# Kernel tuning notes

Measured on AMD Instinct MI355X. Metric: run time of the kernel, lower is better.

The kernel has to match this reference:

```python
import jax, jax.numpy as jnp
import numpy as np
from jax import lax

S, B, XD, AD, ZD, K, H = 128, 32, 1024, 8, 4, 3, 50
CN = 32 * 3 * 3
DN = ('NCHW', 'OIHW', 'NCHW')


def setup_inputs():
    key = jax.random.key(0)
    ks = jax.random.split(key, 20)
    g = lambda k, sh, s=0.1: jax.random.normal(k, sh, dtype=jnp.float32) * s
    z = lambda n: jnp.zeros((n,), jnp.float32)
    return {
        'x': jax.random.uniform(ks[0], (S, B, XD), dtype=jnp.float32),
        'eps': jax.random.normal(ks[1], (S, B, AD), dtype=jnp.float32),
        'Wc0': g(ks[2], (32, 1, 3, 3)), 'bc0': z(32),
        'Wc1': g(ks[3], (32, 32, 3, 3)), 'bc1': z(32),
        'Wc2': g(ks[4], (32, 32, 3, 3)), 'bc2': z(32),
        'Wm': g(ks[5], (AD, CN)), 'bm': z(AD),
        'Wlv': g(ks[6], (AD, CN)), 'blv': z(AD),
        'Wd': g(ks[7], (CN, AD)), 'bd': z(CN),
        'Wt0': g(ks[8], (32, 32, 3, 3)), 'bt0': z(32),
        'Wt1': g(ks[9], (32, 32, 3, 3)), 'bt1': z(32),
        'Wt2': g(ks[10], (32, 32, 3, 3)), 'bt2': z(32),
        'Wg': g(ks[11], (32, 1, 1, 1)), 'bg': z(1),
        'A': jnp.tile(jnp.eye(ZD, dtype=jnp.float32)[None], (K, 1, 1)),
        'Bm': g(ks[12], (K, ZD, AD), 0.05),
        'Cm': g(ks[13], (K, AD, ZD), 0.05),
        'a_init': jnp.zeros((1, AD), jnp.float32),
        'W_ih': g(ks[14], (4 * H, AD)), 'W_hh': g(ks[15], (4 * H, H)),
        'b_ih': z(4 * H), 'b_hh': z(4 * H),
        'Wa': g(ks[16], (K, H)), 'ba': z(K),
    }


def _conv(h, W, b):
    y = lax.conv_general_dilated(h, W, (2, 2), 'VALID', dimension_numbers=DN)
    return y + b[None, :, None, None]


def _convT(h, W, b, op):
    # PyTorch ConvTranspose2d(k=3, stride=2, padding=0, output_padding=op)
    Wf = jnp.transpose(jnp.flip(W, (2, 3)), (1, 0, 2, 3))
    pad = (2, 2 + op)
    y = lax.conv_general_dilated(h, Wf, (1, 1), [pad, pad], lhs_dilation=(2, 2), dimension_numbers=DN)
    return y + b[None, :, None, None]


def _forward(x, eps, Wc0, bc0, Wc1, bc1, Wc2, bc2, Wm, bm, Wlv, blv, Wd, bd,
             Wt0, bt0, Wt1, bt1, Wt2, bt2, Wg, bg, A, Bm, Cm, a_init,
             W_ih, W_hh, b_ih, b_hh, Wa, ba):
    relu, sig = jax.nn.relu, jax.nn.sigmoid
    # ---- encode: x -> a ----
    xf = x.reshape(S * B, 1, 32, 32)
    h = relu(_conv(xf, Wc0, bc0))          # (SB,32,15,15)
    h = relu(_conv(h, Wc1, bc1))           # (SB,32,7,7)
    h = relu(_conv(h, Wc2, bc2))           # (SB,32,3,3)
    feat = h.reshape(S, B, CN)
    a_mean = feat @ Wm.T + bm
    a_logvar = sig(feat @ Wlv.T + blv)
    a = a_mean + eps * jnp.exp(0.5 * a_logvar)
    # ---- decode: a -> log_y ----
    d = (a.reshape(S * B, AD) @ Wd.T + bd).reshape(S * B, 32, 3, 3)
    d = relu(_convT(d, Wt0, bt0, 0))       # (SB,32,7,7)
    d = relu(_convT(d, Wt1, bt1, 0))       # (SB,32,15,15)
    d = relu(_convT(d, Wt2, bt2, 1))       # (SB,32,32,32)
    log_y = sig(jnp.einsum('nchw,c->nhw', d, Wg[:, 0, 0, 0]) + bg[0]).reshape(S, B, XD)
    # ---- alpha from a_{t-1} via LSTM ----
    a_tm1 = jnp.concatenate([jnp.broadcast_to(a_init[:, None, :], (1, B, AD)), a[:-1]], 0)
    def lstm_step(carry, xt):
        h_, c_ = carry
        gates = xt @ W_ih.T + b_ih + h_ @ W_hh.T + b_hh
        i, f, gg, o = jnp.split(gates, 4, axis=-1)
        c_ = sig(f) * c_ + sig(i) * jnp.tanh(gg)
        h_ = sig(o) * jnp.tanh(c_)
        return (h_, c_), h_
    _, hs = lax.scan(lstm_step, (jnp.zeros((B, H), jnp.float32), jnp.zeros((B, H), jnp.float32)), a_tm1)
    alpha = jax.nn.softmax(hs @ Wa.T + ba, axis=-1)     # (S,B,K)
    A_mix = jnp.einsum('sbk,kij->sbij', alpha, A)
    B_mix = jnp.einsum('sbk,kij->sbij', alpha, Bm)
    C_mix = jnp.einsum('sbk,kij->sbij', alpha, Cm)
    u = a_tm1
    # ---- Kalman filter ----
    Qm = 0.08 * jnp.eye(ZD, dtype=jnp.float32)
    Rm = 0.03 * jnp.eye(AD, dtype=jnp.float32)
    Iz = jnp.eye(ZD, dtype=jnp.float32)
    mu0 = jnp.zeros((B, ZD), jnp.float32)
    Sigma0 = 20.0 * jnp.tile(Iz[None], (B, 1, 1))
    def filt(carry, xs):
        mu, Sig = carry
        A_t, B_t, C_t, a_t, u_t, first = xs
        mu_p = jnp.einsum('bij,bj->bi', A_t, mu) + jnp.einsum('bij,bj->bi', B_t, u_t)
        Sig_p = A_t @ Sig @ jnp.swapaxes(A_t, 1, 2) + Qm
        mu_p = jnp.where(first, mu0, mu_p)
        Sig_p = jnp.where(first, Sigma0, Sig_p)
        res = a_t - jnp.einsum('bij,bj->bi', C_t, mu_p)
        S_ = C_t @ Sig_p @ jnp.swapaxes(C_t, 1, 2) + Rm
        Kt = Sig_p @ jnp.swapaxes(C_t, 1, 2) @ jnp.linalg.inv(S_)
        mu_f = mu_p + jnp.einsum('bij,bj->bi', Kt, res)
        IKC = Iz - Kt @ C_t
        Sig_f = IKC @ Sig_p @ jnp.swapaxes(IKC, 1, 2) + Kt @ Rm @ jnp.swapaxes(Kt, 1, 2)
        return (mu_f, Sig_f), (mu_p, mu_f, Sig_p, Sig_f)
    first = jnp.arange(S) == 0
    _, (mu_pred, mu_filt, Sig_pred, Sig_filt) = lax.scan(filt, (mu0, Sigma0), (A_mix, B_mix, C_mix, a, u, first))
    # ---- RTS smoother ----
    def smooth(carry, xs):
        mu_s, Sig_s = carry
        Sf, A_n, Sp_n, muf, muf_n = xs
        J = Sf @ jnp.swapaxes(A_n, 1, 2) @ jnp.linalg.inv(Sp_n)
        mu_new = muf + jnp.einsum('bij,bj->bi', J, mu_s - muf_n)
        Sig_new = Sf + J @ (Sig_s - Sp_n) @ jnp.swapaxes(J, 1, 2)
        return (mu_new, Sig_new), (mu_new, Sig_new)
    _, (mu_sm, Sig_sm) = lax.scan(smooth, (mu_filt[-1], Sig_filt[-1]),
                                  (Sig_filt[:-1], A_mix[1:], Sig_pred[1:], mu_filt[:-1], mu_filt[1:]),
                                  reverse=True)
    mu_smooth = jnp.concatenate([mu_sm, mu_filt[-1:]], 0)
    Sigma_smooth = jnp.concatenate([Sig_sm, Sig_filt[-1:]], 0)
    return log_y, a, a_mean, a_logvar, mu_smooth, Sigma_smooth


def reference(x, eps, Wc0, bc0, Wc1, bc1, Wc2, bc2, Wm, bm, Wlv, blv, Wd, bd,
              Wt0, bt0, Wt1, bt1, Wt2, bt2, Wg, bg, A, Bm, Cm, a_init,
              W_ih, W_hh, b_ih, b_hh, Wa, ba):
    return _forward(x, eps, Wc0, bc0, Wc1, bc1, Wc2, bc2, Wm, bm, Wlv, blv, Wd, bd,
                    Wt0, bt0, Wt1, bt1, Wt2, bt2, Wg, bg, A, Bm, Cm, a_init,
                    W_ih, W_hh, b_ih, b_hh, Wa, ba)
```

## Files before the change

### kernel.cpp

```cpp
#include <hip/hip_runtime.h>
#include <math.h>

#define DI __device__ __forceinline__

DI float sigm(float x){ return 1.0f/(1.0f+__expf(-x)); }
DI float tanhx(float x){ float ax=fabsf(x); float e=__expf(2.0f*ax); float t=1.0f-2.0f/(e+1.0f); return copysignf(t,x); }
DI unsigned short f2bf(float x){ unsigned u=__float_as_uint(x); return (unsigned short)((u+0x7fffu+((u>>16)&1u))>>16); }

typedef __attribute__((ext_vector_type(8))) short bf16x8;
typedef __attribute__((ext_vector_type(4))) float f32x4;
#define MFMA16(a,b,c) __builtin_amdgcn_mfma_f32_16x16x32_bf16(a,b,c,0,0,0)

static constexpr int RS  = 296;
static constexpr int RSZ = 9472;
static constexpr int AS  = 40;

static constexpr size_t OFF_A   = 4194304;
static constexpr size_t OFF_AM  = OFF_A   + 32768;
static constexpr size_t OFF_ALV = OFF_AM  + 32768;
static constexpr size_t OFF_MU  = OFF_ALV + 32768;
static constexpr size_t OFF_SG  = OFF_MU  + 16384;

DI float inv4_lane(float Mv, int r, int c){
  int a0=(c==0)?1:0, a1=(c<=1)?2:1, a2=(c<=2)?3:2;
  int b0=(r==0)?1:0, b1=(r<=1)?2:1, b2=(r<=2)?3:2;
  float m00=__shfl(Mv,(a0<<3)|b0,64), m01=__shfl(Mv,(a0<<3)|b1,64), m02=__shfl(Mv,(a0<<3)|b2,64);
  float m10=__shfl(Mv,(a1<<3)|b0,64), m11=__shfl(Mv,(a1<<3)|b1,64), m12=__shfl(Mv,(a1<<3)|b2,64);
  float m20=__shfl(Mv,(a2<<3)|b0,64), m21=__shfl(Mv,(a2<<3)|b1,64), m22=__shfl(Mv,(a2<<3)|b2,64);
  float det3 = m00*(m11*m22-m12*m21) - m01*(m10*m22-m12*m20) + m02*(m10*m21-m11*m20);
  float adj = (((r+c)&1)? -det3 : det3);
  float det=0.f;
  #pragma unroll
  for(int i=0;i<4;i++)
    det += __shfl(Mv,(i<<3),64)*__shfl(adj,i,64);
  return adj*(1.0f/det);
}

DI void inv4_serial(const float* m, float* o){
  float i0 = m[5]*m[10]*m[15]-m[5]*m[11]*m[14]-m[9]*m[6]*m[15]+m[9]*m[7]*m[14]+m[13]*m[6]*m[11]-m[13]*m[7]*m[10];
  float i4 = -m[4]*m[10]*m[15]+m[4]*m[11]*m[14]+m[8]*m[6]*m[15]-m[8]*m[7]*m[14]-m[12]*m[6]*m[11]+m[12]*m[7]*m[10];
  float i8 = m[4]*m[9]*m[15]-m[4]*m[11]*m[13]-m[8]*m[5]*m[15]+m[8]*m[7]*m[13]+m[12]*m[5]*m[11]-m[12]*m[7]*m[9];
  float i12= -m[4]*m[9]*m[14]+m[4]*m[10]*m[13]+m[8]*m[5]*m[14]-m[8]*m[6]*m[13]-m[12]*m[5]*m[10]+m[12]*m[6]*m[9];
  float i1 = -m[1]*m[10]*m[15]+m[1]*m[11]*m[14]+m[9]*m[2]*m[15]-m[9]*m[3]*m[14]-m[13]*m[2]*m[11]+m[13]*m[3]*m[10];
  float i5 = m[0]*m[10]*m[15]-m[0]*m[11]*m[14]-m[8]*m[2]*m[15]+m[8]*m[3]*m[14]+m[12]*m[2]*m[11]-m[12]*m[3]*m[10];
  float i9 = -m[0]*m[9]*m[15]+m[0]*m[11]*m[13]+m[8]*m[1]*m[15]-m[8]*m[3]*m[13]-m[12]*m[1]*m[11]+m[12]*m[3]*m[9];
  float i13= m[0]*m[9]*m[14]-m[0]*m[10]*m[13]-m[8]*m[1]*m[14]+m[8]*m[2]*m[13]+m[12]*m[1]*m[10]-m[12]*m[2]*m[9];
  float i2 = m[1]*m[6]*m[15]-m[1]*m[7]*m[14]-m[5]*m[2]*m[15]+m[5]*m[3]*m[14]+m[13]*m[2]*m[7]-m[13]*m[3]*m[6];
  float i6 = -m[0]*m[6]*m[15]+m[0]*m[7]*m[14]+m[4]*m[2]*m[15]-m[4]*m[3]*m[14]-m[12]*m[2]*m[7]+m[12]*m[3]*m[6];
  float i10= m[0]*m[5]*m[15]-m[0]*m[7]*m[13]-m[4]*m[1]*m[15]+m[4]*m[3]*m[13]+m[12]*m[1]*m[7]-m[12]*m[3]*m[5];
  float i14= -m[0]*m[5]*m[14]+m[0]*m[6]*m[13]+m[4]*m[1]*m[14]-m[4]*m[2]*m[13]-m[12]*m[1]*m[6]+m[12]*m[2]*m[5];
  float i3 = -m[1]*m[6]*m[11]+m[1]*m[7]*m[10]+m[5]*m[2]*m[11]-m[5]*m[3]*m[10]-m[9]*m[2]*m[7]+m[9]*m[3]*m[6];
  float i7 = m[0]*m[6]*m[11]-m[0]*m[7]*m[10]-m[4]*m[2]*m[11]+m[4]*m[3]*m[10]+m[8]*m[2]*m[7]-m[8]*m[3]*m[6];
  float i11= -m[0]*m[5]*m[11]+m[0]*m[7]*m[9]+m[4]*m[1]*m[11]-m[4]*m[3]*m[9]-m[8]*m[1]*m[7]+m[8]*m[3]*m[5];
  float i15= m[0]*m[5]*m[10]-m[0]*m[6]*m[9]-m[4]*m[1]*m[10]+m[4]*m[2]*m[9]+m[8]*m[1]*m[6]-m[8]*m[2]*m[5];
  float rd=1.0f/(m[0]*i0+m[1]*i4+m[2]*i8+m[3]*i12);
  o[0]=i0*rd; o[1]=i1*rd; o[2]=i2*rd; o[3]=i3*rd;
  o[4]=i4*rd; o[5]=i5*rd; o[6]=i6*rd; o[7]=i7*rd;
  o[8]=i8*rd; o[9]=i9*rd; o[10]=i10*rd; o[11]=i11*rd;
  o[12]=i12*rd; o[13]=i13*rd; o[14]=i14*rd; o[15]=i15*rd;
}

__global__ __launch_bounds__(256) void k_prep(
    const float* __restrict__ Wc1, const float* __restrict__ Wc2,
    const float* __restrict__ Wt0, const float* __restrict__ Wt1, const float* __restrict__ Wt2,
    unsigned short* __restrict__ ws16)
{
  int idx = blockIdx.x*256 + threadIdx.x;
  int mat = idx/RSZ, rem = idx%RSZ;
  int co = rem/RS, t = rem%RS;
  float v = 0.f;
  if (t < 288){
    int tap = t>>5, ci = t&31;
    if      (mat==0) v = Wc1[co*288+ci*9+tap];
    else if (mat==1) v = Wc2[co*288+ci*9+tap];
    else if (mat==2) v = Wt0[ci*288+co*9+tap];
    else if (mat==3) v = Wt1[ci*288+co*9+tap];
    else             v = Wt2[ci*288+co*9+tap];
  }
  ws16[idx] = f2bf(v);
}

struct EncSh {
  alignas(16) float img[1024];
  alignas(16) unsigned short h0T[9040];
  alignas(16) unsigned short h1T[2000];
  alignas(16) unsigned short BT1e[9472];
  alignas(16) unsigned short BT2e[9472];
  alignas(16) float feat[288];
};

__global__ __launch_bounds__(256) void k_enc(
    const float* __restrict__ x, const float* __restrict__ eps,
    const float* __restrict__ Wc0, const float* __restrict__ bc0,
    const float* __restrict__ bc1, const float* __restrict__ bc2,
    const float* __restrict__ Wm, const float* __restrict__ bm,
    const float* __restrict__ Wlv, const float* __restrict__ blv,
    const unsigned short* __restrict__ ws16,
    float* __restrict__ out)
{
  __shared__ EncSh E;
  const int n = blockIdx.x, tid = threadIdx.x;
  const int lane = tid & 63, wave = tid >> 6, g = lane >> 4, c15 = lane & 15;

  for (int i=tid;i<1024;i+=256) E.img[i]=x[(size_t)n*1024+i];
  {
    uint4* dst=(uint4*)E.BT1e;
    const uint4* src=(const uint4*)ws16;
    for (int i=tid;i<2368;i+=256) dst[i]=src[i];
  }
  if (tid<32){ E.h0T[225*AS+tid]=0; E.h1T[49*AS+tid]=0; }
  __syncthreads();

  for (int i=tid;i<7200;i+=256){
    int co=i&31, p=i>>5, oy=p/15, ox=p%15;
    float acc=bc0[co];
    const float* wp=Wc0+co*9;
    int base=2*oy*32+2*ox;
    #pragma unroll
    for(int ky=0;ky<3;ky++)
      #pragma unroll
      for(int kx=0;kx<3;kx++)
        acc += E.img[base+ky*32+kx]*wp[ky*3+kx];
    E.h0T[p*AS+co]=f2bf(fmaxf(acc,0.0f));
  }
  __syncthreads();

  {
    const int mt=wave;
    const int oy=mt*2+(c15>>3), ox=c15&7;
    f32x4 acc0={0.f,0.f,0.f,0.f}, acc1={0.f,0.f,0.f,0.f};
    #pragma unroll 1
    for (int ky=0;ky<3;ky++){
      #pragma unroll
      for (int kx=0;kx<3;kx++){
        int iy=2*oy+ky, ix=2*ox+kx;
        int pix=(iy<15&&ix<15)?(iy*15+ix):225;
        bf16x8 af=*(const bf16x8*)&E.h0T[pix*AS+g*8];
        int tap=ky*3+kx;
        bf16x8 b0=*(const bf16x8*)&E.BT1e[c15*RS+tap*32+g*8];
        bf16x8 b1=*(const bf16x8*)&E.BT1e[(c15+16)*RS+tap*32+g*8];
        acc0=MFMA16(af,b0,acc0);
        acc1=MFMA16(af,b1,acc1);
      }
    }
    float bA=bc1[c15], bB=bc1[c15+16];
    #pragma unroll
    for (int r=0;r<4;r++){
      int p16=g*4+r, oy2=mt*2+(p16>>3), ox2=p16&7;
      if (oy2<7 && ox2<7){
        E.h1T[(oy2*7+ox2)*AS+c15]   =f2bf(fmaxf(acc0[r]+bA,0.f));
        E.h1T[(oy2*7+ox2)*AS+c15+16]=f2bf(fmaxf(acc1[r]+bB,0.f));
      }
    }
  }
  __syncthreads();

  if (wave<2){
    const int nt=wave;
    const int valid=(c15<9);
    const int oy=c15/3, ox=c15-oy*3;
    f32x4 acc={0.f,0.f,0.f,0.f};
    #pragma unroll 1
    for (int ky=0;ky<3;ky++){
      #pragma unroll
      for (int kx=0;kx<3;kx++){
        int pix=valid?((2*oy+ky)*7+(2*ox+kx)):49;
        bf16x8 af=*(const bf16x8*)&E.h1T[pix*AS+g*8];
        int tap=ky*3+kx;
        bf16x8 bfr=*(const bf16x8*)&E.BT2e[(nt*16+c15)*RS+tap*32+g*8];
        acc=MFMA16(af,bfr,acc);
      }
    }
    float bb=bc2[nt*16+c15];
    #pragma unroll
    for (int r=0;r<4;r++){
      int p16=g*4+r;
      if (p16<9) E.feat[(nt*16+c15)*9+p16]=fmaxf(acc[r]+bb,0.f);
    }
  }
  __syncthreads();

  if (tid<64){
    const int j=tid>>3, kk=tid&7;
    float s1=0.f,s2=0.f;
    const float* wm=Wm+j*288;
    const float* wl=Wlv+j*288;
    #pragma unroll 6
    for(int m=kk*36;m<kk*36+36;m++){ float f=E.feat[m]; s1+=f*wm[m]; s2+=f*wl[m]; }
    #pragma unroll
    for(int d=4;d>0;d>>=1){ s1+=__shfl_down(s1,d,64); s2+=__shfl_down(s2,d,64); }
    if(kk==0){
      size_t o=(size_t)n*8+j;
      float am=s1+bm[j];
      float lv=sigm(s2+blv[j]);
      float av=am+eps[o]*__expf(0.5f*lv);
      out[OFF_AM+o]=am;
      out[OFF_ALV+o]=lv;
      out[OFF_A+o]=av;
    }
  }
}

struct DecSh {
  alignas(16) float aa[8];
  alignas(16) unsigned short d0T[400];
  alignas(16) unsigned short t0T[2000];
  alignas(16) unsigned short t1T[9040];
  alignas(16) unsigned short BT0[9472];
  alignas(16) unsigned short BT1[9472];
  alignas(16) unsigned short BT2[9472];
};
struct SeqSh {
  alignas(16) float a_loc[1024];
  alignas(16) float a0[8];
  alignas(16) float h[56];
  float gates[200];
  float logit[4];
  float alpha[384];
  float muf[512];
  float Sigf[2048];
  float Sigp[2048];
  float Jb[2048];
  float Amat[48];
  float Bmat[96];
  float Cmat[96];
  float gram[96];
  float mcb[16];
  float zb[4];
  float bub[4];
  float zk[1536];
  float Buk[1536];
};
union MainSh { DecSh d; SeqSh q; };

DI void kf_help(SeqSh& Q, int hs, int hidx){
  float al0=Q.alpha[hs*3+0], al1=Q.alpha[hs*3+1], al2=Q.alpha[hs*3+2];
  if (hidx<16){
    Q.mcb[hidx]= al0*al0*Q.gram[hidx]    + al1*al1*Q.gram[16+hidx] + al2*al2*Q.gram[32+hidx]
               + al0*al1*Q.gram[48+hidx] + al0*al2*Q.gram[64+hidx] + al1*al2*Q.gram[80+hidx];
  } else if (hidx<20){
    int i=hidx-16;
    Q.zb[i]=al0*Q.zk[hs*12+i]+al1*Q.zk[hs*12+4+i]+al2*Q.zk[hs*12+8+i];
  } else if (hidx<24){
    int i=hidx-20;
    Q.bub[i]=al0*Q.Buk[hs*12+i]+al1*Q.Buk[hs*12+4+i]+al2*Q.Buk[hs*12+8+i];
  }
}

DI void kf_step2(SeqSh& Q, int ks, int r, int c, bool aid,
                 float& mu0, float& mu1, float& mu2, float& mu3, float& Sg)
{
  float mp0,mp1,mp2,mp3, Sp;
  if (aid){
    mp0=mu0+Q.bub[0]; mp1=mu1+Q.bub[1]; mp2=mu2+Q.bub[2]; mp3=mu3+Q.bub[3];
    Sp=Sg+((r==c)?0.08f:0.f);
  } else {
    float al0=Q.alpha[ks*3+0], al1=Q.alpha[ks*3+1], al2=Q.alpha[ks*3+2];
    int e=((r&3)<<2)|(c&3);
    float At=al0*Q.Amat[e]+al1*Q.Amat[16+e]+al2*Q.Amat[32+e];
    float mcc=(c==0)?mu0:((c==1)?mu1:((c==2)?mu2:((c==3)?mu3:0.f)));
    float qv=(c<4)?At*mcc:0.f;
    qv+=__shfl_xor(qv,1,64); qv+=__shfl_xor(qv,2,64);
    float rowv=qv+Q.bub[r&3];
    mp0=__shfl(rowv,0,64); mp1=__shfl(rowv,8,64); mp2=__shfl(rowv,16,64); mp3=__shfl(rowv,24,64);
    float T=0.f;
    #pragma unroll
    for(int k=0;k<4;k++) T+=__shfl(At,(r<<3)|k,64)*__shfl(Sg,(k<<3)|c,64);
    float sp=0.f;
    #pragma unroll
    for(int k=0;k<4;k++) sp+=__shfl(T,(r<<3)|k,64)*__shfl(At,(c<<3)|k,64);
    Sp=sp+((r==c)?0.08f:0.f);
  }
  if (ks==0){ mp0=0.f;mp1=0.f;mp2=0.f;mp3=0.f; Sp=(r==c)?20.f:0.f; }
  if (r<4&&c<4) Q.Sigp[ks*16+r*4+c]=Sp;
  float w0=Q.zb[0]-(Q.mcb[0]*mp0 +Q.mcb[1]*mp1 +Q.mcb[2]*mp2 +Q.mcb[3]*mp3);
  float w1=Q.zb[1]-(Q.mcb[4]*mp0 +Q.mcb[5]*mp1 +Q.mcb[6]*mp2 +Q.mcb[7]*mp3);
  float w2=Q.zb[2]-(Q.mcb[8]*mp0 +Q.mcb[9]*mp1 +Q.mcb[10]*mp2+Q.mcb[11]*mp3);
  float w3=Q.zb[3]-(Q.mcb[12]*mp0+Q.mcb[13]*mp1+Q.mcb[14]*mp2+Q.mcb[15]*mp3);
  float gv=(r==c)?1.f:0.f;
  #pragma unroll
  for(int k=0;k<4;k++)
    gv+=__shfl(Sp,(r<<3)|k,64)*Q.mcb[(k<<2)|(c&3)]*(1.0f/0.03f);
  float Gi=inv4_lane(gv,r,c);
  float Sf=0.f;
  #pragma unroll
  for(int k=0;k<4;k++) Sf+=__shfl(Gi,(r<<3)|k,64)*__shfl(Sp,(k<<3)|c,64);
  if (r<4&&c<4) Q.Sigf[ks*16+r*4+c]=Sf;
  float wc=(c==0)?w0:((c==1)?w1:((c==2)?w2:w3));
  float p=(c<4)?Sf*wc:0.f;
  p+=__shfl_xor(p,1,64); p+=__shfl_xor(p,2,64);
  float mpr=(r==0)?mp0:((r==1)?mp1:((r==2)?mp2:mp3));
  float mufr=mpr+p*(1.0f/0.03f);
  if (r<4&&c==0) Q.muf[ks*4+r]=mufr;
  mu0=__shfl(mufr,0,64); mu1=__shfl(mufr,8,64); mu2=__shfl(mufr,16,64); mu3=__shfl(mufr,24,64);
  Sg=Sf;
}

__global__ __launch_bounds__(512) void k_main(
    const float* __restrict__ Wd, const float* __restrict__ bd,
    const float* __restrict__ bt0, const float* __restrict__ bt1, const float* __restrict__ bt2,
    const float* __restrict__ Wg, const float* __restrict__ bgp,
    const float* __restrict__ Ag, const float* __restrict__ Bg, const float* __restrict__ Cg,
    const float* __restrict__ a_init,
    const float* __restrict__ W_ih, const float* __restrict__ W_hh,
    const float* __restrict__ b_ih, const float* __restrict__ b_hh,
    const float* __restrict__ Wa, const float* __restrict__ ba,
    const unsigned short* __restrict__ ws16,
    float* __restrict__ out)
{
  __shared__ MainSh sh;
  const int tid=threadIdx.x;
  const float* aglob = out + OFF_A;

  if (blockIdx.x < 32){
    if (tid>=320) return;
    SeqSh& Q = sh.q;
    const int b=blockIdx.x;
    for (int i=tid;i<1024;i+=320){ int s=i>>3, j=i&7; Q.a_loc[i]=aglob[((size_t)s*32+b)*8+j]; }
    if (tid<8)  Q.a0[tid]=a_init[tid];
    if (tid<56) Q.h[tid]=0.f;
    for (int i=tid;i<48;i+=320) Q.Amat[i]=Ag[i];
    for (int i=tid;i<96;i+=320){ Q.Bmat[i]=Bg[i]; Q.Cmat[i]=Cg[i]; }

    const int gr = tid-64;
    float wr[52], wi[8], bsum=0.f, creg=0.f;
    if (tid>=64 && tid<264){
      #pragma unroll
      for(int k=0;k<50;k++) wr[k]=W_hh[gr*50+k];
      wr[50]=0.f; wr[51]=0.f;
      #pragma unroll
      for(int j=0;j<8;j++) wi[j]=W_ih[gr*8+j];
      bsum=b_ih[gr]+b_hh[gr];
    }
    float wl[52]; float bl=0.f;
    if (tid>=264 && tid<267){
      #pragma unroll
      for(int k=0;k<50;k++) wl[k]=Wa[(tid-264)*50+k];
      wl[50]=0.f; wl[51]=0.f;
      bl=ba[tid-264];
    }
    const int r=tid>>3, c=tid&7;
    float mu0=0.f,mu1=0.f,mu2=0.f,mu3=0.f, Sg=0.f;
    bool aid=false;
    if (tid<64){
      int ok=1;
      if (r<4&&c<4){
        float d=(r==c)?1.f:0.f;
        ok=(Ag[r*4+c]==d)&&(Ag[16+r*4+c]==d)&&(Ag[32+r*4+c]==d);
      }
      aid=(bool)__all(ok);
    }
    __syncthreads();
    if (tid<96){
      int which=tid>>4, e=tid&15, i2=e>>2, j2=e&3;
      float s2=0.f;
      if (which<3){
        const float* C=&Q.Cmat[which*32];
        #pragma unroll
        for(int m=0;m<8;m++) s2+=C[m*4+i2]*C[m*4+j2];
      } else {
        int k2=(which==5)?1:0, l2=(which==3)?1:2;
        const float* Ck=&Q.Cmat[k2*32];
        const float* Cl=&Q.Cmat[l2*32];
        #pragma unroll
        for(int m=0;m<8;m++) s2+=Ck[m*4+i2]*Cl[m*4+j2]+Cl[m*4+i2]*Ck[m*4+j2];
      }
      Q.gram[tid]=s2;
    }
    for (int idx=tid; idx<1536; idx+=320){
      int s=idx/12, r2=idx-s*12, k=r2>>2, i=r2&3;
      const float* Crow=&Q.Cmat[k*32];
      const float* Brow=&Q.Bmat[k*32+i*8];
      const float* av=&Q.a_loc[s*8];
      const float* uv=(s==0)?Q.a0:&Q.a_loc[(s-1)*8];
      float z2=0.f, bu=0.f;
      #pragma unroll
      for(int m=0;m<8;m++){ z2+=Crow[m*4+i]*av[m]; bu+=Brow[m]*uv[m]; }
      Q.zk[idx]=z2; Q.Buk[idx]=bu;
    }
    __syncthreads();

    for (int s=0;s<128;s++){
      if (tid>=64 && tid<264){
        const float* ap=(s==0)?Q.a0:(Q.a_loc+(s-1)*8);
        float4 av0=*(const float4*)ap, av1=*(const float4*)(ap+4);
        float aA=bsum+av0.x*wi[0]+av0.y*wi[1]+av0.z*wi[2]+av0.w*wi[3]
                     +av1.x*wi[4]+av1.y*wi[5]+av1.z*wi[6]+av1.w*wi[7];
        float aB=0.f,aC=0.f,aD=0.f;
        #pragma unroll
        for(int q=0;q<13;q++){
          float4 hv=*(const float4*)&Q.h[4*q];
          aA+=hv.x*wr[4*q]; aB+=hv.y*wr[4*q+1]; aC+=hv.z*wr[4*q+2]; aD+=hv.w*wr[4*q+3];
        }
        Q.gates[gr]=(aA+aB)+(aC+aD);
      } else if (tid>=264 && tid<267){
        if (s>0){
          float aA=bl,aB=0.f,aC=0.f,aD=0.f;
          #pragma unroll
          for(int q=0;q<13;q++){
            float4 hv=*(const float4*)&Q.h[4*q];
            aA+=hv.x*wl[4*q]; aB+=hv.y*wl[4*q+1]; aC+=hv.z*wl[4*q+2]; aD+=hv.w*wl[4*q+3];
          }
          Q.logit[tid-264]=(aA+aB)+(aC+aD);
        }
      } else if (tid>=267 && tid<291 && s>=2){
        kf_help(Q,s-2,tid-267);
      }
      __syncthreads();
      if (tid>=64 && tid<114){
        int j=gr;
        float ig=sigm(Q.gates[j]);
        float fg=sigm(Q.gates[50+j]);
        float gg=tanhx(Q.gates[100+j]);
        float og=sigm(Q.gates[150+j]);
        creg=fg*creg+ig*gg;
        Q.h[j]=og*tanhx(creg);
      } else if (tid>=114 && tid<117 && s>0){
        int j=tid-114;
        float l0=Q.logit[0], l1=Q.logit[1], l2=Q.logit[2];
        float mx=fmaxf(l0,fmaxf(l1,l2));
        float e0=__expf(l0-mx), e1=__expf(l1-mx), e2=__expf(l2-mx);
        float lj=(j==0)?l0:((j==1)?l1:l2);
        Q.alpha[(s-1)*3+j]=__expf(lj-mx)/(e0+e1+e2);
      } else if (tid<64 && s>=2){
        kf_step2(Q,s-2,r,c,aid,mu0,mu1,mu2,mu3,Sg);
      }
      __syncthreads();
    }
    if (tid>=264 && tid<267){
      float aA=bl,aB=0.f,aC=0.f,aD=0.f;
      #pragma unroll
      for(int q=0;q<13;q++){
        float4 hv=*(const float4*)&Q.h[4*q];
        aA+=hv.x*wl[4*q]; aB+=hv.y*wl[4*q+1]; aC+=hv.z*wl[4*q+2]; aD+=hv.w*wl[4*q+3];
      }
      Q.logit[tid-264]=(aA+aB)+(aC+aD);
    } else if (tid>=267 && tid<291){
      kf_help(Q,126,tid-267);
    }
    __syncthreads();
    if (tid>=64 && tid<67){
      int j=tid-64;
      float l0=Q.logit[0], l1=Q.logit[1], l2=Q.logit[2];
      float mx=fmaxf(l0,fmaxf(l1,l2));
      float e0=__expf(l0-mx), e1=__expf(l1-mx), e2=__expf(l2-mx);
      float lj=(j==0)?l0:((j==1)?l1:l2);
      Q.alpha[127*3+j]=__expf(lj-mx)/(e0+e1+e2);
    } else if (tid<64){
      kf_step2(Q,126,r,c,aid,mu0,mu1,mu2,mu3,Sg);
    }
    __syncthreads();
    if (tid>=267 && tid<291) kf_help(Q,127,tid-267);
    __syncthreads();
    if (tid<64) kf_step2(Q,127,r,c,aid,mu0,mu1,mu2,mu3,Sg);
    __syncthreads();
    if (tid<127){
      const int n2=tid;
      float al0=Q.alpha[(n2+1)*3+0], al1=Q.alpha[(n2+1)*3+1], al2=Q.alpha[(n2+1)*3+2];
      float An[16], Sp[16], Spi[16], Sf[16], T[16];
      #pragma unroll
      for(int k=0;k<16;k++){
        An[k]=al0*Q.Amat[k]+al1*Q.Amat[16+k]+al2*Q.Amat[32+k];
        Sp[k]=Q.Sigp[(n2+1)*16+k];
        Sf[k]=Q.Sigf[n2*16+k];
      }
      inv4_serial(Sp,Spi);
      #pragma unroll
      for(int r2=0;r2<4;r2++)
        #pragma unroll
        for(int c2=0;c2<4;c2++){
          float s2=0.f;
          #pragma unroll
          for(int k=0;k<4;k++) s2+=Sf[r2*4+k]*An[c2*4+k];
          T[r2*4+c2]=s2;
        }
      #pragma unroll
      for(int r2=0;r2<4;r2++)
        #pragma unroll
        for(int c2=0;c2<4;c2++){
          float s2=0.f;
          #pragma unroll
          for(int k=0;k<4;k++) s2+=T[r2*4+k]*Spi[k*4+c2];
          Q.Jb[n2*16+r2*4+c2]=s2;
        }
    }
    __syncthreads();
    if (tid<64){
      const bool act=(r<4&&c<4);
      if (r<4&&c==0) out[OFF_MU+((size_t)127*32+b)*4+r]=Q.muf[127*4+r];
      if (act)       out[OFF_SG+((size_t)127*32+b)*16+r*4+c]=Q.Sigf[127*16+r*4+c];
      float ms0=Q.muf[508], ms1=Q.muf[509], ms2=Q.muf[510], ms3=Q.muf[511];
      float Ss=act?Q.Sigf[127*16+r*4+c]:0.f;
      for (int n2=126;n2>=0;n2--){
        float Jv =act?Q.Jb[n2*16+r*4+c]:0.f;
        float Sfv=act?Q.Sigf[n2*16+r*4+c]:0.f;
        float Spn=act?Q.Sigp[(n2+1)*16+r*4+c]:0.f;
        float Dv=Ss-Spn;
        float T2=0.f;
        #pragma unroll
        for(int k=0;k<4;k++) T2+=__shfl(Jv,(r<<3)|k,64)*__shfl(Dv,(k<<3)|c,64);
        float Sn=Sfv;
        #pragma unroll
        for(int k=0;k<4;k++) Sn+=__shfl(T2,(r<<3)|k,64)*__shfl(Jv,(c<<3)|k,64);
        float msc=(c==0)?ms0:((c==1)?ms1:((c==2)?ms2:ms3));
        float dmc=(c<4)?(msc-Q.muf[(n2+1)*4+(c&3)]):0.f;
        float p=Jv*dmc;
        p+=__shfl_xor(p,1,64); p+=__shfl_xor(p,2,64);
        float mun=Q.muf[n2*4+(r&3)]+p;
        if (r<4&&c==0) out[OFF_MU+((size_t)n2*32+b)*4+r]=mun;
        if (act)       out[OFF_SG+((size_t)n2*32+b)*16+r*4+c]=Sn;
        ms0=__shfl(mun,0,64); ms1=__shfl(mun,8,64); ms2=__shfl(mun,16,64); ms3=__shfl(mun,24,64);
        Ss=Sn;
      }
    }
    return;
  }

  DecSh& D = sh.d;
  const int n = blockIdx.x - 32;
  const int lane = tid & 63, wave = tid >> 6, g = lane >> 4, c15 = lane & 15;

  if (tid<8) D.aa[tid]=aglob[(size_t)n*8+tid];
  {
    uint4* dst=(uint4*)D.BT0;
    const uint4* src=(const uint4*)(ws16 + 2*RSZ);
    for (int i=tid;i<3552;i+=512) dst[i]=src[i];
  }
  if (tid<32){ D.d0T[9*AS+tid]=0; D.t0T[49*AS+tid]=0; D.t1T[225*AS+tid]=0; }
  __syncthreads();
  if (tid<288){
    float acc=bd[tid];
    #pragma unroll
    for(int j=0;j<8;j++) acc+=D.aa[j]*Wd[tid*8+j];
    D.d0T[(tid%9)*AS+(tid/9)]=f2bf(acc);
  }
  __syncthreads();
  {
    const int mt=wave>>1, nt=wave&1;
    const int pa=mt*16+c15;
    const int oh=pa/7, ow=pa%7;
    const bool pv=(pa<49);
    f32x4 acc={0.f,0.f,0.f,0.f};
    #pragma unroll 1
    for (int kh=0;kh<3;kh++){
      int th=oh-kh;
      bool vh=pv && th>=0 && !(th&1) && th<=4;
      int ihb=(th>>1)*3;
      #pragma unroll
      for (int kw=0;kw<3;kw++){
        int tw=ow-kw;
        bool v=vh && tw>=0 && !(tw&1) && tw<=4;
        int pix=v?(ihb+(tw>>1)):9;
        bf16x8 af=*(const bf16x8*)&D.d0T[pix*AS+g*8];
        int tap=kh*3+kw;
        bf16x8 bb=*(const bf16x8*)&D.BT0[(nt*16+c15)*RS+tap*32+g*8];
        acc=MFMA16(af,bb,acc);
      }
    }
    float bz=bt0[nt*16+c15];
    #pragma unroll
    for (int r=0;r<4;r++){
      int pc=mt*16+g*4+r;
      if (pc<49) D.t0T[pc*AS+nt*16+c15]=f2bf(fmaxf(acc[r]+bz,0.f));
    }
  }
  __syncthreads();
  {
    float bA=bt1[c15], bB=bt1[c15+16];
    #pragma unroll 1
    for (int u2=0;u2<2;u2++){
      int unit=wave+u2*8;
      int cls=unit>>2, mt=unit&3;
      int ph=cls>>1, pw=cls&1;
      int ii=mt*2+(c15>>3), jj=c15&7;
      f32x4 acc0={0.f,0.f,0.f,0.f}, acc1={0.f,0.f,0.f,0.f};
      #pragma unroll 1
      for (int kh=ph;kh<3;kh+=2){
        int ih=ii-(kh>>1);
        #pragma unroll
        for (int kw=pw;kw<3;kw+=2){
          int iw=jj-(kw>>1);
          int pix=(ih>=0&&ih<7&&iw>=0&&iw<7)?(ih*7+iw):49;
          bf16x8 af=*(const bf16x8*)&D.t0T[pix*AS+g*8];
          int tap=kh*3+kw;
          bf16x8 b0=*(const bf16x8*)&D.BT1[c15*RS+tap*32+g*8];
          bf16x8 b1=*(const bf16x8*)&D.BT1[(c15+16)*RS+tap*32+g*8];
          acc0=MFMA16(af,b0,acc0);
          acc1=MFMA16(af,b1,acc1);
        }
      }
      #pragma unroll
      for (int r=0;r<4;r++){
        int p16=g*4+r;
        int iio=mt*2+(p16>>3), jjo=p16&7;
        int oh=2*iio+ph, ow=2*jjo+pw;
        if (oh<15 && ow<15){
          D.t1T[(oh*15+ow)*AS+c15]   =f2bf(fmaxf(acc0[r]+bA,0.f));
          D.t1T[(oh*15+ow)*AS+c15+16]=f2bf(fmaxf(acc1[r]+bB,0.f));
        }
      }
    }
  }
  __syncthreads();
  {
    float bt2a=bt2[c15], bt2b=bt2[c15+16], wga=Wg[c15], wgb=Wg[c15+16], bgv=bgp[0];
    #pragma unroll 1
    for (int u2=0;u2<2;u2++){
      int ii=wave+u2*8;
      #pragma unroll 1
      for (int cls=0;cls<4;cls++){
        int ph=cls>>1, pw=cls&1;
        f32x4 acc0={0.f,0.f,0.f,0.f}, acc1={0.f,0.f,0.f,0.f};
        #pragma unroll 1
        for (int kh=ph;kh<3;kh+=2){
          int ih=ii-(kh>>1);
          if (ih<0||ih>14) continue;
          #pragma unroll
          for (int kw=pw;kw<3;kw+=2){
            int iw=c15-(kw>>1);
            int pix=(iw>=0&&iw<15)?(ih*15+iw):225;
            bf16x8 af=*(const bf16x8*)&D.t1T[pix*AS+g*8];
            int tap=kh*3+kw;
            bf16x8 b0=*(const bf16x8*)&D.BT2[c15*RS+tap*32+g*8];
            bf16x8 b1=*(const bf16x8*)&D.BT2[(c15+16)*RS+tap*32+g*8];
            acc0=MFMA16(af,b0,acc0);
            acc1=MFMA16(af,b1,acc1);
          }
        }
        int oh=2*ii+ph;
        float s0=fmaxf(acc0[0]+bt2a,0.f)*wga+fmaxf(acc1[0]+bt2b,0.f)*wgb;
        float s1=fmaxf(acc0[1]+bt2a,0.f)*wga+fmaxf(acc1[1]+bt2b,0.f)*wgb;
        float s2=fmaxf(acc0[2]+bt2a,0.f)*wga+fmaxf(acc1[2]+bt2b,0.f)*wgb;
        float s3=fmaxf(acc0[3]+bt2a,0.f)*wga+fmaxf(acc1[3]+bt2b,0.f)*wgb;
        #pragma unroll
        for (int d=1;d<16;d<<=1){
          s0+=__shfl_xor(s0,d,64); s1+=__shfl_xor(s1,d,64);
          s2+=__shfl_xor(s2,d,64); s3+=__shfl_xor(s3,d,64);
        }
        if (c15==0){
          size_t ob=(size_t)n*1024+(size_t)oh*32+pw;
          out[ob+2*(g*4+0)]=sigm(s0+bgv);
          out[ob+2*(g*4+1)]=sigm(s1+bgv);
          out[ob+2*(g*4+2)]=sigm(s2+bgv);
          out[ob+2*(g*4+3)]=sigm(s3+bgv);
        }
      }
    }
  }
}

extern "C" void kernel_launch(void* const* d_in, const int* in_sizes, int n_in,
                              void* d_out, int out_size, void* d_ws, size_t ws_size,
                              hipStream_t stream)
{
  const float* x    =(const float*)d_in[0];
  const float* eps  =(const float*)d_in[1];
  const float* Wc0  =(const float*)d_in[2];
  const float* bc0  =(const float*)d_in[3];
  const float* Wc1  =(const float*)d_in[4];
  const float* bc1  =(const float*)d_in[5];
  const float* Wc2  =(const float*)d_in[6];
  const float* bc2  =(const float*)d_in[7];
  const float* Wm   =(const float*)d_in[8];
  const float* bm   =(const float*)d_in[9];
  const float* Wlv  =(const float*)d_in[10];
  const float* blv  =(const float*)d_in[11];
  const float* Wd   =(const float*)d_in[12];
  const float* bd   =(const float*)d_in[13];
  const float* Wt0  =(const float*)d_in[14];
  const float* bt0  =(const float*)d_in[15];
  const float* Wt1  =(const float*)d_in[16];
  const float* bt1  =(const float*)d_in[17];
  const float* Wt2  =(const float*)d_in[18];
  const float* bt2  =(const float*)d_in[19];
  const float* Wg   =(const float*)d_in[20];
  const float* bg   =(const float*)d_in[21];
  const float* A    =(const float*)d_in[22];
  const float* Bm   =(const float*)d_in[23];
  const float* Cm   =(const float*)d_in[24];
  const float* a0   =(const float*)d_in[25];
  const float* W_ih =(const float*)d_in[26];
  const float* W_hh =(const float*)d_in[27];
  const float* b_ih =(const float*)d_in[28];
  const float* b_hh =(const float*)d_in[29];
  const float* Wa   =(const float*)d_in[30];
  const float* ba   =(const float*)d_in[31];
  float* out=(float*)d_out;
  unsigned short* ws16=(unsigned short*)d_ws;

  k_prep<<<185,256,0,stream>>>(Wc1,Wc2,Wt0,Wt1,Wt2,ws16);
  k_enc<<<4096,256,0,stream>>>(x,eps,Wc0,bc0,bc1,bc2,Wm,bm,Wlv,blv,ws16,out);
  k_main<<<4128,512,0,stream>>>(Wd,bd,bt0,bt1,bt2,Wg,bg,A,Bm,Cm,a0,
                                W_ih,W_hh,b_ih,b_hh,Wa,ba,ws16,out);
}
```

Measured before the change: 332.7 us.

## Run Kalman filter as standalone loop after LSTM scan with precomputed mixtures

```diff
diff --git a/kernel.cpp b/kernel.cpp
--- a/kernel.cpp
+++ b/kernel.cpp
@@ -225,76 +225,12 @@
   float Bmat[96];
   float Cmat[96];
   float gram[96];
-  float mcb[16];
-  float zb[4];
-  float bub[4];
   float zk[1536];
   float Buk[1536];
+  float mca[2048];
+  float zbu[1024];
 };
 union MainSh { DecSh d; SeqSh q; };
-
-DI void kf_help(SeqSh& Q, int hs, int hidx){
-  float al0=Q.alpha[hs*3+0], al1=Q.alpha[hs*3+1], al2=Q.alpha[hs*3+2];
-  if (hidx<16){
-    Q.mcb[hidx]= al0*al0*Q.gram[hidx]    + al1*al1*Q.gram[16+hidx] + al2*al2*Q.gram[32+hidx]
-               + al0*al1*Q.gram[48+hidx] + al0*al2*Q.gram[64+hidx] + al1*al2*Q.gram[80+hidx];
-  } else if (hidx<20){
-    int i=hidx-16;
-    Q.zb[i]=al0*Q.zk[hs*12+i]+al1*Q.zk[hs*12+4+i]+al2*Q.zk[hs*12+8+i];
-  } else if (hidx<24){
-    int i=hidx-20;
-    Q.bub[i]=al0*Q.Buk[hs*12+i]+al1*Q.Buk[hs*12+4+i]+al2*Q.Buk[hs*12+8+i];
-  }
-}
-
-DI void kf_step2(SeqSh& Q, int ks, int r, int c, bool aid,
-                 float& mu0, float& mu1, float& mu2, float& mu3, float& Sg)
-{
-  float mp0,mp1,mp2,mp3, Sp;
-  if (aid){
-    mp0=mu0+Q.bub[0]; mp1=mu1+Q.bub[1]; mp2=mu2+Q.bub[2]; mp3=mu3+Q.bub[3];
-    Sp=Sg+((r==c)?0.08f:0.f);
-  } else {
-    float al0=Q.alpha[ks*3+0], al1=Q.alpha[ks*3+1], al2=Q.alpha[ks*3+2];
-    int e=((r&3)<<2)|(c&3);
-    float At=al0*Q.Amat[e]+al1*Q.Amat[16+e]+al2*Q.Amat[32+e];
-    float mcc=(c==0)?mu0:((c==1)?mu1:((c==2)?mu2:((c==3)?mu3:0.f)));
-    float qv=(c<4)?At*mcc:0.f;
-    qv+=__shfl_xor(qv,1,64); qv+=__shfl_xor(qv,2,64);
-    float rowv=qv+Q.bub[r&3];
-    mp0=__shfl(rowv,0,64); mp1=__shfl(rowv,8,64); mp2=__shfl(rowv,16,64); mp3=__shfl(rowv,24,64);
-    float T=0.f;
-    #pragma unroll
-    for(int k=0;k<4;k++) T+=__shfl(At,(r<<3)|k,64)*__shfl(Sg,(k<<3)|c,64);
-    float sp=0.f;
-    #pragma unroll
-    for(int k=0;k<4;k++) sp+=__shfl(T,(r<<3)|k,64)*__shfl(At,(c<<3)|k,64);
-    Sp=sp+((r==c)?0.08f:0.f);
-  }
-  if (ks==0){ mp0=0.f;mp1=0.f;mp2=0.f;mp3=0.f; Sp=(r==c)?20.f:0.f; }
-  if (r<4&&c<4) Q.Sigp[ks*16+r*4+c]=Sp;
-  float w0=Q.zb[0]-(Q.mcb[0]*mp0 +Q.mcb[1]*mp1 +Q.mcb[2]*mp2 +Q.mcb[3]*mp3);
-  float w1=Q.zb[1]-(Q.mcb[4]*mp0 +Q.mcb[5]*mp1 +Q.mcb[6]*mp2 +Q.mcb[7]*mp3);
-  float w2=Q.zb[2]-(Q.mcb[8]*mp0 +Q.mcb[9]*mp1 +Q.mcb[10]*mp2+Q.mcb[11]*mp3);
-  float w3=Q.zb[3]-(Q.mcb[12]*mp0+Q.mcb[13]*mp1+Q.mcb[14]*mp2+Q.mcb[15]*mp3);
-  float gv=(r==c)?1.f:0.f;
-  #pragma unroll
-  for(int k=0;k<4;k++)
-    gv+=__shfl(Sp,(r<<3)|k,64)*Q.mcb[(k<<2)|(c&3)]*(1.0f/0.03f);
-  float Gi=inv4_lane(gv,r,c);
-  float Sf=0.f;
-  #pragma unroll
-  for(int k=0;k<4;k++) Sf+=__shfl(Gi,(r<<3)|k,64)*__shfl(Sp,(k<<3)|c,64);
-  if (r<4&&c<4) Q.Sigf[ks*16+r*4+c]=Sf;
-  float wc=(c==0)?w0:((c==1)?w1:((c==2)?w2:w3));
-  float p=(c<4)?Sf*wc:0.f;
-  p+=__shfl_xor(p,1,64); p+=__shfl_xor(p,2,64);
-  float mpr=(r==0)?mp0:((r==1)?mp1:((r==2)?mp2:mp3));
-  float mufr=mpr+p*(1.0f/0.03f);
-  if (r<4&&c==0) Q.muf[ks*4+r]=mufr;
-  mu0=__shfl(mufr,0,64); mu1=__shfl(mufr,8,64); mu2=__shfl(mufr,16,64); mu3=__shfl(mufr,24,64);
-  Sg=Sf;
-}
 
 __global__ __launch_bounds__(512) void k_main(
     const float* __restrict__ Wd, const float* __restrict__ bd,
@@ -314,6 +250,7 @@
 
   if (blockIdx.x < 32){
     if (tid>=320) return;
+    __builtin_amdgcn_s_setprio(1);
     SeqSh& Q = sh.q;
     const int b=blockIdx.x;
     for (int i=tid;i<1024;i+=320){ int s=i>>3, j=i&7; Q.a_loc[i]=aglob[((size_t)s*32+b)*8+j]; }
@@ -340,7 +277,6 @@
       bl=ba[tid-264];
     }
     const int r=tid>>3, c=tid&7;
-    float mu0=0.f,mu1=0.f,mu2=0.f,mu3=0.f, Sg=0.f;
     bool aid=false;
     if (tid<64){
       int ok=1;
@@ -403,8 +339,6 @@
           }
           Q.logit[tid-264]=(aA+aB)+(aC+aD);
         }
-      } else if (tid>=267 && tid<291 && s>=2){
-        kf_help(Q,s-2,tid-267);
       }
       __syncthreads();
       if (tid>=64 && tid<114){
@@ -422,8 +356,6 @@
         float e0=__expf(l0-mx), e1=__expf(l1-mx), e2=__expf(l2-mx);
         float lj=(j==0)?l0:((j==1)?l1:l2);
         Q.alpha[(s-1)*3+j]=__expf(lj-mx)/(e0+e1+e2);
-      } else if (tid<64 && s>=2){
-        kf_step2(Q,s-2,r,c,aid,mu0,mu1,mu2,mu3,Sg);
       }
       __syncthreads();
     }
@@ -435,24 +367,87 @@
         aA+=hv.x*wl[4*q]; aB+=hv.y*wl[4*q+1]; aC+=hv.z*wl[4*q+2]; aD+=hv.w*wl[4*q+3];
       }
       Q.logit[tid-264]=(aA+aB)+(aC+aD);
-    } else if (tid>=267 && tid<291){
-      kf_help(Q,126,tid-267);
     }
     __syncthreads();
-    if (tid>=64 && tid<67){
-      int j=tid-64;
+    if (tid<3){
+      int j=tid;
       float l0=Q.logit[0], l1=Q.logit[1], l2=Q.logit[2];
       float mx=fmaxf(l0,fmaxf(l1,l2));
       float e0=__expf(l0-mx), e1=__expf(l1-mx), e2=__expf(l2-mx);
       float lj=(j==0)?l0:((j==1)?l1:l2);
       Q.alpha[127*3+j]=__expf(lj-mx)/(e0+e1+e2);
-    } else if (tid<64){
-      kf_step2(Q,126,r,c,aid,mu0,mu1,mu2,mu3,Sg);
     }
     __syncthreads();
-    if (tid>=267 && tid<291) kf_help(Q,127,tid-267);
+    for (int idx=tid; idx<2048; idx+=320){
+      int s=idx>>4, e=idx&15;
+      float al0=Q.alpha[s*3+0], al1=Q.alpha[s*3+1], al2=Q.alpha[s*3+2];
+      Q.mca[idx]= al0*al0*Q.gram[e]    + al1*al1*Q.gram[16+e] + al2*al2*Q.gram[32+e]
+                + al0*al1*Q.gram[48+e] + al0*al2*Q.gram[64+e] + al1*al2*Q.gram[80+e];
+    }
+    for (int idx=tid; idx<1024; idx+=320){
+      int s=idx>>3, t=idx&7;
+      float al0=Q.alpha[s*3+0], al1=Q.alpha[s*3+1], al2=Q.alpha[s*3+2];
+      if (t<4) Q.zbu[idx]=al0*Q.zk[s*12+t]+al1*Q.zk[s*12+4+t]+al2*Q.zk[s*12+8+t];
+      else {
+        int i=t-4;
+        Q.zbu[idx]=al0*Q.Buk[s*12+i]+al1*Q.Buk[s*12+4+i]+al2*Q.Buk[s*12+8+i];
+      }
+    }
     __syncthreads();
-    if (tid<64) kf_step2(Q,127,r,c,aid,mu0,mu1,mu2,mu3,Sg);
+    if (tid<64){
+      const bool act=(r<4&&c<4);
+      const int cc=c&3, rr4=r&3;
+      float mu0=0.f,mu1=0.f,mu2=0.f,mu3=0.f, Sg=0.f;
+      for (int s3=0;s3<128;s3++){
+        const float* mrow=&Q.mca[s3*16+cc*4];
+        float mr0=mrow[0], mr1=mrow[1], mr2=mrow[2], mr3=mrow[3];
+        float mc0=Q.mca[s3*16+cc], mc1=Q.mca[s3*16+4+cc], mc2=Q.mca[s3*16+8+cc], mc3=Q.mca[s3*16+12+cc];
+        float zc=Q.zbu[s3*8+cc];
+        float bu0=Q.zbu[s3*8+4], bu1=Q.zbu[s3*8+5], bu2=Q.zbu[s3*8+6], bu3=Q.zbu[s3*8+7];
+        float mp0,mp1,mp2,mp3, Sp;
+        if (aid){
+          mp0=mu0+bu0; mp1=mu1+bu1; mp2=mu2+bu2; mp3=mu3+bu3;
+          Sp=Sg+((r==c)?0.08f:0.f);
+        } else {
+          float al0=Q.alpha[s3*3+0], al1=Q.alpha[s3*3+1], al2=Q.alpha[s3*3+2];
+          int e2=(rr4<<2)|cc;
+          float At=al0*Q.Amat[e2]+al1*Q.Amat[16+e2]+al2*Q.Amat[32+e2];
+          float mcc=(c==0)?mu0:((c==1)?mu1:((c==2)?mu2:((c==3)?mu3:0.f)));
+          float qv=(c<4)?At*mcc:0.f;
+          qv+=__shfl_xor(qv,1,64); qv+=__shfl_xor(qv,2,64);
+          float bur=(rr4==0)?bu0:((rr4==1)?bu1:((rr4==2)?bu2:bu3));
+          float rowv=qv+bur;
+          mp0=__shfl(rowv,0,64); mp1=__shfl(rowv,8,64); mp2=__shfl(rowv,16,64); mp3=__shfl(rowv,24,64);
+          float T=0.f;
+          #pragma unroll
+          for(int k=0;k<4;k++) T+=__shfl(At,(r<<3)|k,64)*__shfl(Sg,(k<<3)|c,64);
+          float sp=0.f;
+          #pragma unroll
+          for(int k=0;k<4;k++) sp+=__shfl(T,(r<<3)|k,64)*__shfl(At,(c<<3)|k,64);
+          Sp=sp+((r==c)?0.08f:0.f);
+        }
+        if (s3==0){ mp0=0.f;mp1=0.f;mp2=0.f;mp3=0.f; Sp=(r==c)?20.f:0.f; }
+        if (act) Q.Sigp[s3*16+rr4*4+cc]=Sp;
+        float wc=zc-(mr0*mp0+mr1*mp1+mr2*mp2+mr3*mp3);
+        float gv=(r==c)?1.f:0.f;
+        gv+=__shfl(Sp,(r<<3)|0,64)*mc0*(1.0f/0.03f);
+        gv+=__shfl(Sp,(r<<3)|1,64)*mc1*(1.0f/0.03f);
+        gv+=__shfl(Sp,(r<<3)|2,64)*mc2*(1.0f/0.03f);
+        gv+=__shfl(Sp,(r<<3)|3,64)*mc3*(1.0f/0.03f);
+        float Gi=inv4_lane(gv,r,c);
+        float Sf=0.f;
+        #pragma unroll
+        for(int k=0;k<4;k++) Sf+=__shfl(Gi,(r<<3)|k,64)*__shfl(Sp,(k<<3)|c,64);
+        if (act) Q.Sigf[s3*16+rr4*4+cc]=Sf;
+        float p=(c<4)?Sf*wc:0.f;
+        p+=__shfl_xor(p,1,64); p+=__shfl_xor(p,2,64);
+        float mpr=(r==0)?mp0:((r==1)?mp1:((r==2)?mp2:mp3));
+        float mufr=mpr+p*(1.0f/0.03f);
+        if (r<4&&c==0) Q.muf[s3*4+r]=mufr;
+        mu0=__shfl(mufr,0,64); mu1=__shfl(mufr,8,64); mu2=__shfl(mufr,16,64); mu3=__shfl(mufr,24,64);
+        Sg=Sf;
+      }
+    }
     __syncthreads();
     if (tid<127){
       const int n2=tid;
```

Result: faster. 312.9 us (-6.0%).
